# Performance work log

Measured on AMD Instinct MI355X. Metric: run time of the kernel, lower is better.

## Reference

```python
import jax, jax.numpy as jnp
import numpy as np

C = 64          # channel multiplicity of node irreps (64x0e + 64x1o)
N = 10000       # nodes
E = 160000      # edges
F_EDGE = 8      # edge radial features (8x0e)
N_ELEM = 10     # one-hot element types (node_attrs, unused by this block)
WNUM = 4 * C    # conv_tp.weight_numel: 4 uvu instructions x 64 channels
SQ3 = float(np.sqrt(3.0))


def split_feats(x):
    # e3nn flat layout: [64 scalars | 64 vectors x 3 (u-major)]
    s = x[:, :C]
    v = x[:, C:].reshape(-1, C, 3)
    return s, v


def o3_linear(s, v, W0, W1):
    # per-irrep channel mixing with 1/sqrt(fan_in) normalization
    inv = 1.0 / float(np.sqrt(C))
    return (s @ W0) * inv, jnp.einsum('ncm,cd->ndm', v, W1) * inv


def fc_net(x, ws):
    # e3nn FullyConnectedNet: silu MLP with 1/sqrt(fan_in) scaling, no act on last
    for w in ws[:-1]:
        x = jax.nn.silu((x @ w) / float(np.sqrt(w.shape[0])))
    w = ws[-1]
    return (x @ w) / float(np.sqrt(w.shape[0]))


def setup_inputs() -> dict:
    key = jax.random.key(0)
    ks = jax.random.split(key, 16)
    inp = {}
    inp['node_attrs'] = jax.random.normal(ks[0], (N, N_ELEM), jnp.float32)
    inp['node_feats'] = jax.random.normal(ks[1], (N, C + 3 * C), jnp.float32)
    inp['edge_attrs'] = jax.random.normal(ks[2], (E, 4), jnp.float32)
    inp['edge_feats'] = jax.random.normal(ks[3], (E, F_EDGE), jnp.float32)
    inp['edge_index'] = jax.random.randint(ks[4], (2, E), 0, N, jnp.int32)
    inp['edge_vectors'] = jax.random.normal(ks[5], (E, 3), jnp.float32)
    inp['batch'] = jax.random.randint(ks[6], (N,), 0, 16, jnp.int32)
    inp['num_graphs'] = 16
    # learned params
    inp['W1_0'] = jax.random.normal(ks[7], (C, C), jnp.float32)
    inp['W1_1'] = jax.random.normal(ks[8], (C, C), jnp.float32)
    inp['W2_0'] = jax.random.normal(ks[9], (C, C), jnp.float32)
    inp['W2_1'] = jax.random.normal(ks[10], (C, C), jnp.float32)
    inp['fc_w0'] = jax.random.normal(ks[11], (F_EDGE, 64), jnp.float32)
    inp['fc_w1'] = jax.random.normal(ks[12], (64, 64), jnp.float32)
    inp['fc_w2'] = jax.random.normal(ks[13], (64, 64), jnp.float32)
    inp['fc_w3'] = jax.random.normal(ks[14], (64, WNUM), jnp.float32)
    k15, k16 = jax.random.split(ks[15])
    inp['Wf'] = jax.random.normal(k15, (2 * C, 1), jnp.float32)   # 128x0e mid -> 1x0e
    inp['Wm1'] = jax.random.normal(k16, (C, 1), jnp.float32)      # 64x1o -> 1x1o multipole
    return inp


def reference(node_attrs, node_feats, edge_attrs, edge_feats, edge_index,
              edge_vectors, batch, num_graphs,
              W1_0, W1_1, W2_0, W2_1, fc_w0, fc_w1, fc_w2, fc_w3, Wf, Wm1):
    sender = edge_index[0]
    receiver = edge_index[1]

    # per-edge tensor-product weights from radial features: [E, 4*C]
    tp_w = fc_net(edge_feats, [fc_w0, fc_w1, fc_w2, fc_w3])
    w0, w1, w2, w3 = (tp_w[:, 0 * C:1 * C], tp_w[:, 1 * C:2 * C],
                      tp_w[:, 2 * C:3 * C], tp_w[:, 3 * C:4 * C])

    s, v = split_feats(node_feats)
    s1, v1 = o3_linear(s, v, W1_0, W1_1)
    s2, v2 = o3_linear(s, v, W2_0, W2_1)

    # gather + symmetric bond features
    bs = s1[sender] + s2[receiver]          # [E, C] scalars
    bv = v1[sender] + v2[receiver]          # [E, C, 3] vectors

    y0 = edge_attrs[:, 0]                   # l=0 edge attr
    y1 = edge_attrs[:, 1:4]                 # l=1 edge attr

    # CG tensor product (uvu, shared_weights=False): only scalar (0e) outputs of
    # irreps_mid reach the final 1x0e o3.Linear, so the 1o paths drop out exactly.
    m0a = w0 * bs * y0[:, None]                                  # 0e x 0e -> 0e
    m0b = w3 * (jnp.einsum('ecm,em->ec', bv, y1) / SQ3)          # 1o x 1o -> 0e

    # final o3.Linear (128x0e -> 1x0e) and /40 scaling
    mid0 = jnp.concatenate([m0a, m0b], axis=-1)                  # [E, 2C]
    p_ji = (mid0 @ Wf)[:, 0] / float(np.sqrt(2 * C)) / 40.0      # [E]

    # double scatter-sum: antisymmetric charge transfer
    charges = (jax.ops.segment_sum(p_ji, receiver, num_segments=N)
               - jax.ops.segment_sum(p_ji, sender, num_segments=N))

    # multipole block: 0e component zeroed then overwritten by charges
    mvec = jnp.einsum('ncm,cd->ndm', v, Wm1)[:, 0, :] / float(np.sqrt(C))  # [N, 3]
    multipoles = jnp.concatenate([charges[:, None], mvec], axis=-1)        # [N, 4]

    return multipoles, p_ji[:, None]
```

## Files before the change

### kernel.cpp

```cpp
#include <hip/hip_runtime.h>
#include <hip/hip_bf16.h>

typedef float v4f __attribute__((ext_vector_type(4)));
typedef float f32x4 __attribute__((ext_vector_type(4)));
typedef unsigned short u16;
typedef unsigned short us4 __attribute__((ext_vector_type(4)));
typedef unsigned short us8 __attribute__((ext_vector_type(8)));
typedef short s16x8 __attribute__((ext_vector_type(8)));

#define N_NODES 10000
#define N_EDGES 160000

#define SWZ(idx, row) ((idx) ^ (((row) & 7) << 3))
#define GIDX(r, o) (((r) << 8) + (((((o) >> 3) ^ ((r) & 7))) << 3) + ((o) & 7))

__device__ __forceinline__ u16 f2b(float x) {
  union { float f; unsigned u; } v; v.f = x;
  unsigned r = v.u + 0x7fffu + ((v.u >> 16) & 1u);
  return (u16)(r >> 16);
}
__device__ __forceinline__ float b2f(u16 u) {
  union { unsigned u; float f; } v; v.u = ((unsigned)u) << 16; return v.f;
}
__device__ __forceinline__ float silu_f(float x) { return x / (1.0f + __expf(-x)); }

__device__ __forceinline__ void bar_lgkm() {
  asm volatile("s_waitcnt lgkmcnt(0)" ::: "memory");
  __builtin_amdgcn_s_barrier();
}

__device__ __forceinline__ void gload_lds16(const u16* g, u16* l) {
  __builtin_amdgcn_global_load_lds(
      (const __attribute__((address_space(1))) unsigned int*)g,
      (__attribute__((address_space(3))) unsigned int*)l, 16, 0, 0);
}

__global__ __launch_bounds__(256) void prep_kernel(
    const float* __restrict__ fcw1, const float* __restrict__ fcw2,
    const float* __restrict__ fcw3,
    const float* __restrict__ W10, const float* __restrict__ W20,
    const float* __restrict__ W11, const float* __restrict__ W21,
    u16* __restrict__ prep, float* __restrict__ out)
{
  const int fid = blockIdx.x * 256 + threadIdx.x;
  for (int i = fid; i < N_NODES; i += 4096) out[(size_t)i * 4] = 0.f;
  int f, sec;
  if (fid < 512)       { sec = 0; f = fid; }
  else if (fid < 1024) { sec = 1; f = fid - 512; }
  else if (fid < 2048) { sec = 2; f = fid - 1024; }
  else if (fid < 3072) { sec = 3; f = fid - 2048; }
  else                 { sec = 4; f = fid - 3072; }
  const int lane = f & 63, kw = (f >> 6) & 1, ut = f >> 7;
  us8 vals;
  #pragma unroll
  for (int j = 0; j < 8; ++j) {
    const int k = kw * 32 + (lane >> 4) * 8 + j;
    float v;
    if (sec == 0) v = fcw1[k * 64 + ut * 16 + (lane & 15)];
    else if (sec == 1) v = fcw2[k * 64 + ut * 16 + (lane & 15)];
    else if (sec == 2) {
      const int col = (ut < 4) ? (ut * 16 + (lane & 15)) : (192 + (ut - 4) * 16 + (lane & 15));
      v = fcw3[k * 256 + col];
    } else if (sec == 3) {
      const int u = ut * 16 + (lane & 15);
      v = (u < 64) ? W10[k * 64 + u] : W20[k * 64 + (u - 64)];
    } else {
      const int u = ut * 16 + (lane & 15);
      v = (u < 64) ? W11[k * 64 + u] : W21[k * 64 + (u - 64)];
    }
    vals[j] = f2b(v);
  }
  *(us8*)&prep[(size_t)fid * 8] = vals;
}

__global__ __launch_bounds__(256) void node_kernel(
    const float* __restrict__ nf,
    const u16* __restrict__ prepNS, const u16* __restrict__ prepNV,
    const float* __restrict__ Wm1,
    u16* __restrict__ Atab, u16* __restrict__ Btab, float* __restrict__ out)
{
  __shared__ u16 Ss[1024];
  __shared__ u16 Vs[3][1024];
  const int tid = threadIdx.x, w = tid >> 6, lane = tid & 63;
  const int nb = blockIdx.x;

  #pragma unroll
  for (int it = 0; it < 4; ++it) {
    const int flat = it * 1024 + tid * 4;
    const int nl = flat >> 8;
    const int col = flat & 255;
    const v4f x = *(const v4f*)&nf[((size_t)(nb * 16 + nl)) * 256 + col];
    #pragma unroll
    for (int i = 0; i < 4; ++i) {
      const int c2 = col + i;
      const u16 b = f2b(x[i]);
      if (c2 < 64) Ss[SWZ(nl * 64 + c2, nl)] = b;
      else {
        const int cc = c2 - 64, c = cc / 3, m = cc - c * 3;
        Vs[m][SWZ(nl * 64 + c, nl)] = b;
      }
    }
  }
  __syncthreads();

  const int nr = lane & 15, kg = (lane >> 4) * 8;
  const u16* plane = (w == 0) ? Ss : Vs[w - 1];
  const u16* pw = (w == 0) ? prepNS : prepNV;
  const s16x8 b0 = *(const s16x8*)&plane[SWZ(nr * 64 + kg, nr)];
  const s16x8 b1 = *(const s16x8*)&plane[SWZ(nr * 64 + 32 + kg, nr)];
  const int node = nb * 16 + nr;
  #pragma unroll
  for (int utg = 0; utg < 8; ++utg) {
    const s16x8 a0 = *(const s16x8*)&pw[((utg * 2 + 0) * 64 + lane) * 8];
    const s16x8 a1 = *(const s16x8*)&pw[((utg * 2 + 1) * 64 + lane) * 8];
    f32x4 acc = {0.f, 0.f, 0.f, 0.f};
    acc = __builtin_amdgcn_mfma_f32_16x16x32_bf16(a0, b0, acc, 0, 0, 0);
    acc = __builtin_amdgcn_mfma_f32_16x16x32_bf16(a1, b1, acc, 0, 0, 0);
    us4 st;
    #pragma unroll
    for (int j = 0; j < 4; ++j) st[j] = f2b(acc[j] * 0.125f);
    u16* tab = (utg < 4) ? Atab : Btab;
    const int ch = w * 64 + (utg & 3) * 16 + (lane >> 4) * 4;
    *(us4*)&tab[(size_t)node * 256 + ch] = st;
  }

  if (tid < 48) {
    const int nl3 = tid / 3, m = tid - nl3 * 3;
    float acc = 0.f;
    #pragma unroll 8
    for (int c = 0; c < 64; ++c)
      acc += b2f(Vs[m][SWZ(nl3 * 64 + c, nl3)]) * Wm1[c];
    out[(nb * 16 + nl3) * 4 + 1 + m] = acc * 0.125f;
  }
}

__device__ __forceinline__ void mfma_layer32(const u16* Hin, u16* Hout,
                                             s16x8 a0, s16x8 a1, int w, int lane) {
  const int er = lane & 15, kg = (lane >> 4) * 8;
  #pragma unroll
  for (int et = 0; et < 2; ++et) {
    const int e = et * 16 + er;
    const s16x8 b0 = *(const s16x8*)&Hin[SWZ(e * 64 + kg, e)];
    const s16x8 b1 = *(const s16x8*)&Hin[SWZ(e * 64 + 32 + kg, e)];
    f32x4 acc = {0.f, 0.f, 0.f, 0.f};
    acc = __builtin_amdgcn_mfma_f32_16x16x32_bf16(a0, b0, acc, 0, 0, 0);
    acc = __builtin_amdgcn_mfma_f32_16x16x32_bf16(a1, b1, acc, 0, 0, 0);
    us4 st;
    #pragma unroll
    for (int j = 0; j < 4; ++j) st[j] = f2b(silu_f(acc[j] * 0.125f));
    *(us4*)&Hout[SWZ(e * 64 + w * 16 + (lane >> 4) * 4, e)] = st;
  }
}

__global__ __launch_bounds__(256, 2) void edge_kernel(
    const float* __restrict__ edge_attrs,
    const float* __restrict__ edge_feats,
    const int*   __restrict__ edge_index,
    const float* __restrict__ fcw0,
    const u16*   __restrict__ prep,
    const float* __restrict__ Wf,
    const u16*   __restrict__ Atab, const u16* __restrict__ Btab,
    float* __restrict__ out, float* __restrict__ p_out)
{
  __shared__ u16 G[2][16384];
  __shared__ u16 HA[2048], HB[2048];
  __shared__ float F[256];
  __shared__ float W0L[512];
  __shared__ float yL[4][32];
  __shared__ float Psum[128];

  const int tid = threadIdx.x, w = tid >> 6, lane = tid & 63;
  const int half = lane >> 5, l31 = lane & 31;
  const int er = lane & 15, kg = (lane >> 4) * 8;
  const int cb = w * 16 + (lane >> 4) * 4;
  const int eb0 = blockIdx.x * 128;

  const u16* pL2 = prep;
  const u16* pL3 = prep + 512 * 8;
  const u16* pL4 = prep + 1024 * 8;
  const s16x8 a2_0 = *(const s16x8*)&pL2[((w * 2 + 0) * 64 + lane) * 8];
  const s16x8 a2_1 = *(const s16x8*)&pL2[((w * 2 + 1) * 64 + lane) * 8];
  const s16x8 a3_0 = *(const s16x8*)&pL3[((w * 2 + 0) * 64 + lane) * 8];
  const s16x8 a3_1 = *(const s16x8*)&pL3[((w * 2 + 1) * 64 + lane) * 8];
  const s16x8 as0 = *(const s16x8*)&pL4[((w * 2 + 0) * 64 + lane) * 8];
  const s16x8 as1 = *(const s16x8*)&pL4[((w * 2 + 1) * 64 + lane) * 8];
  const s16x8 av0 = *(const s16x8*)&pL4[(((4 + w) * 2 + 0) * 64 + lane) * 8];
  const s16x8 av1 = *(const s16x8*)&pL4[(((4 + w) * 2 + 1) * 64 + lane) * 8];
  const v4f wfA = *(const v4f*)&Wf[cb];
  v4f wfB = *(const v4f*)&Wf[64 + cb];
  #pragma unroll
  for (int j = 0; j < 4; ++j) wfB[j] *= 0.5773502691896258f;
  W0L[tid] = fcw0[tid]; W0L[256 + tid] = fcw0[256 + tid];

  const u16* tabW = (w < 2) ? Atab : Btab;
  const int  eoff = (w < 2) ? 0 : N_EDGES;

  int nidx[2][8];
  int sndR[2], rcvR[2];
  v4f eaR[2], f0R[2], f1R[2];

  {
    #pragma unroll
    for (int i = 0; i < 8; ++i)
      nidx[0][i] = edge_index[eoff + eb0 + (w & 1) * 16 + 2 * i + half];
    if (tid < 32) {
      sndR[0] = edge_index[eb0 + tid];
      rcvR[0] = edge_index[N_EDGES + eb0 + tid];
      eaR[0] = *(const v4f*)&edge_attrs[(size_t)(eb0 + tid) * 4];
      f0R[0] = *(const v4f*)&edge_feats[(size_t)(eb0 + tid) * 8];
      f1R[0] = *(const v4f*)&edge_feats[(size_t)(eb0 + tid) * 8 + 4];
    }
    asm volatile("s_waitcnt vmcnt(0)" ::: "memory");
    #pragma unroll
    for (int i = 0; i < 8; ++i) {
      const int grow = w * 16 + 2 * i + half;
      const u16* src = tabW + (size_t)nidx[0][i] * 256 + (size_t)((l31 ^ (grow & 7)) << 3);
      gload_lds16(src, &G[0][(w * 16 + 2 * i) * 256]);
    }
    __builtin_amdgcn_sched_barrier(0);
    if (tid < 32) {
      yL[0][tid] = eaR[0][0]; yL[1][tid] = eaR[0][1];
      yL[2][tid] = eaR[0][2]; yL[3][tid] = eaR[0][3];
      #pragma unroll
      for (int k = 0; k < 4; ++k) {
        F[k * 32 + tid] = f0R[0][k]; F[(k + 4) * 32 + tid] = f1R[0][k];
      }
    }
    bar_lgkm();
  }

  #pragma unroll
  for (int t = 0; t < 4; ++t) {
    const int cur = t & 1, nxt = cur ^ 1;
    const int eb = eb0 + t * 32;

    if (t < 3) {
      const int ebn = eb + 32;
      #pragma unroll
      for (int i = 0; i < 8; ++i)
        nidx[nxt][i] = edge_index[eoff + ebn + (w & 1) * 16 + 2 * i + half];
      if (tid < 32) {
        sndR[nxt] = edge_index[ebn + tid];
        rcvR[nxt] = edge_index[N_EDGES + ebn + tid];
        eaR[nxt] = *(const v4f*)&edge_attrs[(size_t)(ebn + tid) * 4];
        f0R[nxt] = *(const v4f*)&edge_feats[(size_t)(ebn + tid) * 8];
        f1R[nxt] = *(const v4f*)&edge_feats[(size_t)(ebn + tid) * 8 + 4];
      }
      __builtin_amdgcn_sched_barrier(0);
    }

    {
      const int u0 = w * 16 + half * 8;
      float acc[8] = {0.f,0.f,0.f,0.f,0.f,0.f,0.f,0.f};
      #pragma unroll
      for (int k = 0; k < 8; ++k) {
        const float fv = F[k * 32 + l31];
        #pragma unroll
        for (int q = 0; q < 2; ++q) {
          const v4f wr = *(const v4f*)&W0L[k * 64 + u0 + q * 4];
          #pragma unroll
          for (int j = 0; j < 4; ++j) acc[q * 4 + j] += fv * wr[j];
        }
      }
      us8 o;
      #pragma unroll
      for (int j = 0; j < 8; ++j) o[j] = f2b(silu_f(acc[j] * 0.35355339059327373f));
      *(us8*)&HA[SWZ(l31 * 64 + u0, l31)] = o;
    }
    bar_lgkm();
    mfma_layer32(HA, HB, a2_0, a2_1, w, lane);
    bar_lgkm();
    mfma_layer32(HB, HA, a3_0, a3_1, w, lane);
    bar_lgkm();

    f32x4 accS[2], accV[2];
    #pragma unroll
    for (int et = 0; et < 2; ++et) {
      const int e = et * 16 + er;
      const s16x8 b0 = *(const s16x8*)&HA[SWZ(e * 64 + kg, e)];
      const s16x8 b1 = *(const s16x8*)&HA[SWZ(e * 64 + 32 + kg, e)];
      f32x4 aS = {0.f,0.f,0.f,0.f}, aV = {0.f,0.f,0.f,0.f};
      aS = __builtin_amdgcn_mfma_f32_16x16x32_bf16(as0, b0, aS, 0, 0, 0);
      aS = __builtin_amdgcn_mfma_f32_16x16x32_bf16(as1, b1, aS, 0, 0, 0);
      aV = __builtin_amdgcn_mfma_f32_16x16x32_bf16(av0, b0, aV, 0, 0, 0);
      aV = __builtin_amdgcn_mfma_f32_16x16x32_bf16(av1, b1, aV, 0, 0, 0);
      accS[et] = aS; accV[et] = aV;
    }

    asm volatile("s_waitcnt vmcnt(0)" ::: "memory");
    if (t < 3) {
      #pragma unroll
      for (int i = 0; i < 8; ++i) {
        const int grow = w * 16 + 2 * i + half;
        const u16* src = tabW + (size_t)nidx[nxt][i] * 256 + (size_t)((l31 ^ (grow & 7)) << 3);
        gload_lds16(src, &G[nxt][(w * 16 + 2 * i) * 256]);
      }
      __builtin_amdgcn_sched_barrier(0);
    }
    __builtin_amdgcn_s_barrier();

    #pragma unroll
    for (int et = 0; et < 2; ++et) {
      const int e = et * 16 + er;
      const int rA = e, rB = 32 + e;
      const us4 As = *(const us4*)&G[cur][GIDX(rA, cb)];
      const us4 Ax = *(const us4*)&G[cur][GIDX(rA, 64 + cb)];
      const us4 Ay = *(const us4*)&G[cur][GIDX(rA, 128 + cb)];
      const us4 Az = *(const us4*)&G[cur][GIDX(rA, 192 + cb)];
      const us4 Bs = *(const us4*)&G[cur][GIDX(rB, cb)];
      const us4 Bx = *(const us4*)&G[cur][GIDX(rB, 64 + cb)];
      const us4 By = *(const us4*)&G[cur][GIDX(rB, 128 + cb)];
      const us4 Bz = *(const us4*)&G[cur][GIDX(rB, 192 + cb)];
      const float y0 = yL[0][e], yx = yL[1][e], yy = yL[2][e], yz = yL[3][e];
      float part = 0.f;
      #pragma unroll
      for (int j = 0; j < 4; ++j) {
        const float bs = b2f(As[j]) + b2f(Bs[j]);
        const float bv = (b2f(Ax[j]) + b2f(Bx[j])) * yx +
                         (b2f(Ay[j]) + b2f(By[j])) * yy +
                         (b2f(Az[j]) + b2f(Bz[j])) * yz;
        part += accS[et][j] * bs * y0 * wfA[j] + accV[et][j] * bv * wfB[j];
      }
      part += __shfl_xor(part, 16);
      part += __shfl_xor(part, 32);
      if (lane < 16) Psum[w * 32 + et * 16 + lane] = part;
    }
    bar_lgkm();
    if (tid < 32) {
      const float p = (Psum[tid] + Psum[32 + tid] + Psum[64 + tid] + Psum[96 + tid])
                      * 2.7621358640766505e-4f;
      p_out[eb + tid] = p;
      atomicAdd(&out[(size_t)rcvR[cur] * 4], p);
      atomicAdd(&out[(size_t)sndR[cur] * 4], -p);
      if (t < 3) {
        yL[0][tid] = eaR[nxt][0]; yL[1][tid] = eaR[nxt][1];
        yL[2][tid] = eaR[nxt][2]; yL[3][tid] = eaR[nxt][3];
        #pragma unroll
        for (int k = 0; k < 4; ++k) {
          F[k * 32 + tid] = f0R[nxt][k]; F[(k + 4) * 32 + tid] = f1R[nxt][k];
        }
      }
    }
    bar_lgkm();
  }
}

extern "C" void kernel_launch(void* const* d_in, const int* in_sizes, int n_in,
                              void* d_out, int out_size, void* d_ws, size_t ws_size,
                              hipStream_t stream) {
  const float* node_feats = (const float*)d_in[1];
  const float* edge_attrs = (const float*)d_in[2];
  const float* edge_feats = (const float*)d_in[3];
  const int*   edge_index = (const int*)d_in[4];
  const float* W10  = (const float*)d_in[8];
  const float* W11  = (const float*)d_in[9];
  const float* W20  = (const float*)d_in[10];
  const float* W21  = (const float*)d_in[11];
  const float* fcw0 = (const float*)d_in[12];
  const float* fcw1 = (const float*)d_in[13];
  const float* fcw2 = (const float*)d_in[14];
  const float* fcw3 = (const float*)d_in[15];
  const float* Wf   = (const float*)d_in[16];
  const float* Wm1  = (const float*)d_in[17];
  float* out = (float*)d_out;

  char* ws = (char*)d_ws;
  u16* Atab = (u16*)ws;
  u16* Btab = (u16*)(ws + 5120000);
  u16* prep = (u16*)(ws + 10240000);

  prep_kernel<<<16, 256, 0, stream>>>(fcw1, fcw2, fcw3, W10, W20, W11, W21,
                                      prep, out);
  node_kernel<<<625, 256, 0, stream>>>(node_feats, prep + 2048 * 8, prep + 3072 * 8,
                                       Wm1, Atab, Btab, out);
  edge_kernel<<<1250, 256, 0, stream>>>(edge_attrs, edge_feats, edge_index,
                                        fcw0, prep, Wf, Atab, Btab,
                                        out, out + 40000);
}
```

Baseline: 153.1 us.

## Single-buffer edge gather LDS to raise occupancy, double tiles per block

The edge kernel's gather buffer goes from double to single buffered, roughly halving its shared memory footprint, and launch bounds are raised from 2 to 3 blocks per CU. The next tile's gather is now issued after the current tile's reads finish instead of overlapping with its MLP. Each block now handles 8 tiles of 32 edges, so the grid shrinks to 625 blocks. The aim is to hide gather latency through occupancy rather than in-block prefetch, at the cost of losing that intra-block overlap and having fewer blocks. The node kernel's multipole dot product is also spread over 4 lanes with shuffle reduction and Wm1 staged in LDS.

```diff
diff --git a/kernel.cpp b/kernel.cpp
--- a/kernel.cpp
+++ b/kernel.cpp
@@ -10,6 +10,7 @@
 
 #define N_NODES 10000
 #define N_EDGES 160000
+#define NTILE 8
 
 #define SWZ(idx, row) ((idx) ^ (((row) & 7) << 3))
 #define GIDX(r, o) (((r) << 8) + (((((o) >> 3) ^ ((r) & 7))) << 3) + ((o) & 7))
@@ -81,9 +82,11 @@
 {
   __shared__ u16 Ss[1024];
   __shared__ u16 Vs[3][1024];
+  __shared__ float wm1s[64];
   const int tid = threadIdx.x, w = tid >> 6, lane = tid & 63;
   const int nb = blockIdx.x;
 
+  if (tid < 64) wm1s[tid] = Wm1[tid];
   #pragma unroll
   for (int it = 0; it < 4; ++it) {
     const int flat = it * 1024 + tid * 4;
@@ -124,13 +127,18 @@
     *(us4*)&tab[(size_t)node * 256 + ch] = st;
   }
 
-  if (tid < 48) {
-    const int nl3 = tid / 3, m = tid - nl3 * 3;
+  if (tid < 192) {
+    const int task = tid >> 2, sub = tid & 3;
+    const int nl3 = task / 3, m = task - nl3 * 3;
     float acc = 0.f;
-    #pragma unroll 8
-    for (int c = 0; c < 64; ++c)
-      acc += b2f(Vs[m][SWZ(nl3 * 64 + c, nl3)]) * Wm1[c];
-    out[(nb * 16 + nl3) * 4 + 1 + m] = acc * 0.125f;
+    #pragma unroll
+    for (int i = 0; i < 16; ++i) {
+      const int c = sub * 16 + i;
+      acc += b2f(Vs[m][SWZ(nl3 * 64 + c, nl3)]) * wm1s[c];
+    }
+    acc += __shfl_xor(acc, 1);
+    acc += __shfl_xor(acc, 2);
+    if (sub == 0) out[(nb * 16 + nl3) * 4 + 1 + m] = acc * 0.125f;
   }
 }
 
@@ -152,7 +160,7 @@
   }
 }
 
-__global__ __launch_bounds__(256, 2) void edge_kernel(
+__global__ __launch_bounds__(256, 3) void edge_kernel(
     const float* __restrict__ edge_attrs,
     const float* __restrict__ edge_feats,
     const int*   __restrict__ edge_index,
@@ -162,7 +170,7 @@
     const u16*   __restrict__ Atab, const u16* __restrict__ Btab,
     float* __restrict__ out, float* __restrict__ p_out)
 {
-  __shared__ u16 G[2][16384];
+  __shared__ u16 G[16384];
   __shared__ u16 HA[2048], HB[2048];
   __shared__ float F[256];
   __shared__ float W0L[512];
@@ -173,7 +181,7 @@
   const int half = lane >> 5, l31 = lane & 31;
   const int er = lane & 15, kg = (lane >> 4) * 8;
   const int cb = w * 16 + (lane >> 4) * 4;
-  const int eb0 = blockIdx.x * 128;
+  const int eb0 = blockIdx.x * (NTILE * 32);
 
   const u16* pL2 = prep;
   const u16* pL3 = prep + 512 * 8;
@@ -215,7 +223,7 @@
     for (int i = 0; i < 8; ++i) {
       const int grow = w * 16 + 2 * i + half;
       const u16* src = tabW + (size_t)nidx[0][i] * 256 + (size_t)((l31 ^ (grow & 7)) << 3);
-      gload_lds16(src, &G[0][(w * 16 + 2 * i) * 256]);
+      gload_lds16(src, &G[(w * 16 + 2 * i) * 256]);
     }
     __builtin_amdgcn_sched_barrier(0);
     if (tid < 32) {
@@ -230,11 +238,11 @@
   }
 
   #pragma unroll
-  for (int t = 0; t < 4; ++t) {
+  for (int t = 0; t < NTILE; ++t) {
     const int cur = t & 1, nxt = cur ^ 1;
     const int eb = eb0 + t * 32;
 
-    if (t < 3) {
+    if (t < NTILE - 1) {
       const int ebn = eb + 32;
       #pragma unroll
       for (int i = 0; i < 8; ++i)
@@ -288,29 +296,20 @@
     }
 
     asm volatile("s_waitcnt vmcnt(0)" ::: "memory");
-    if (t < 3) {
-      #pragma unroll
-      for (int i = 0; i < 8; ++i) {
-        const int grow = w * 16 + 2 * i + half;
-        const u16* src = tabW + (size_t)nidx[nxt][i] * 256 + (size_t)((l31 ^ (grow & 7)) << 3);
-        gload_lds16(src, &G[nxt][(w * 16 + 2 * i) * 256]);
-      }
-      __builtin_amdgcn_sched_barrier(0);
-    }
     __builtin_amdgcn_s_barrier();
 
     #pragma unroll
     for (int et = 0; et < 2; ++et) {
       const int e = et * 16 + er;
       const int rA = e, rB = 32 + e;
-      const us4 As = *(const us4*)&G[cur][GIDX(rA, cb)];
-      const us4 Ax = *(const us4*)&G[cur][GIDX(rA, 64 + cb)];
-      const us4 Ay = *(const us4*)&G[cur][GIDX(rA, 128 + cb)];
-      const us4 Az = *(const us4*)&G[cur][GIDX(rA, 192 + cb)];
-      const us4 Bs = *(const us4*)&G[cur][GIDX(rB, cb)];
-      const us4 Bx = *(const us4*)&G[cur][GIDX(rB, 64 + cb)];
-      const us4 By = *(const us4*)&G[cur][GIDX(rB, 128 + cb)];
-      const us4 Bz = *(const us4*)&G[cur][GIDX(rB, 192 + cb)];
+      const us4 As = *(const us4*)&G[GIDX(rA, cb)];
+      const us4 Ax = *(const us4*)&G[GIDX(rA, 64 + cb)];
+      const us4 Ay = *(const us4*)&G[GIDX(rA, 128 + cb)];
+      const us4 Az = *(const us4*)&G[GIDX(rA, 192 + cb)];
+      const us4 Bs = *(const us4*)&G[GIDX(rB, cb)];
+      const us4 Bx = *(const us4*)&G[GIDX(rB, 64 + cb)];
+      const us4 By = *(const us4*)&G[GIDX(rB, 128 + cb)];
+      const us4 Bz = *(const us4*)&G[GIDX(rB, 192 + cb)];
       const float y0 = yL[0][e], yx = yL[1][e], yy = yL[2][e], yz = yL[3][e];
       float part = 0.f;
       #pragma unroll
@@ -326,13 +325,24 @@
       if (lane < 16) Psum[w * 32 + et * 16 + lane] = part;
     }
     bar_lgkm();
+
+    if (t < NTILE - 1) {
+      #pragma unroll
+      for (int i = 0; i < 8; ++i) {
+        const int grow = w * 16 + 2 * i + half;
+        const u16* src = tabW + (size_t)nidx[nxt][i] * 256 + (size_t)((l31 ^ (grow & 7)) << 3);
+        gload_lds16(src, &G[(w * 16 + 2 * i) * 256]);
+      }
+      __builtin_amdgcn_sched_barrier(0);
+    }
+
     if (tid < 32) {
       const float p = (Psum[tid] + Psum[32 + tid] + Psum[64 + tid] + Psum[96 + tid])
                       * 2.7621358640766505e-4f;
       p_out[eb + tid] = p;
       atomicAdd(&out[(size_t)rcvR[cur] * 4], p);
       atomicAdd(&out[(size_t)sndR[cur] * 4], -p);
-      if (t < 3) {
+      if (t < NTILE - 1) {
         yL[0][tid] = eaR[nxt][0]; yL[1][tid] = eaR[nxt][1];
         yL[2][tid] = eaR[nxt][2]; yL[3][tid] = eaR[nxt][3];
         #pragma unroll
@@ -373,7 +383,7 @@
                                       prep, out);
   node_kernel<<<625, 256, 0, stream>>>(node_feats, prep + 2048 * 8, prep + 3072 * 8,
                                        Wm1, Atab, Btab, out);
-  edge_kernel<<<1250, 256, 0, stream>>>(edge_attrs, edge_feats, edge_index,
-                                        fcw0, prep, Wf, Atab, Btab,
-                                        out, out + 40000);
-}
+  edge_kernel<<<625, 256, 0, stream>>>(edge_attrs, edge_feats, edge_index,
+                                       fcw0, prep, Wf, Atab, Btab,
+                                       out, out + 40000);
+}
```

After: 161.9 us. +5.7%, slower.

## Move first radial MLP layer to MFMA and parallelize multipole dot product

Applied to the files above, without the earlier changes.

Replaces the scalar FMA loop for the first fc_net layer (8->64) with a bf16 MFMA, zero-padding K from 8 to 32. The prep kernel packs fcw0 into the MFMA operand layout, and edge features are staged to LDS as bf16. It also wraps the MFMA sections in s_setprio to favour matrix issue, and splits the node multipole dot product across 4 lanes with shuffle reduction, reading Wm1 from LDS. Rounding the first-layer inputs and weights to bf16 adds some precision loss.

```diff
diff --git a/kernel.cpp b/kernel.cpp
--- a/kernel.cpp
+++ b/kernel.cpp
@@ -36,6 +36,7 @@
 }
 
 __global__ __launch_bounds__(256) void prep_kernel(
+    const float* __restrict__ fcw0,
     const float* __restrict__ fcw1, const float* __restrict__ fcw2,
     const float* __restrict__ fcw3,
     const float* __restrict__ W10, const float* __restrict__ W20,
@@ -43,32 +44,43 @@
     u16* __restrict__ prep, float* __restrict__ out)
 {
   const int fid = blockIdx.x * 256 + threadIdx.x;
-  for (int i = fid; i < N_NODES; i += 4096) out[(size_t)i * 4] = 0.f;
+  for (int i = fid; i < N_NODES; i += 4352) out[(size_t)i * 4] = 0.f;
   int f, sec;
   if (fid < 512)       { sec = 0; f = fid; }
   else if (fid < 1024) { sec = 1; f = fid - 512; }
   else if (fid < 2048) { sec = 2; f = fid - 1024; }
   else if (fid < 3072) { sec = 3; f = fid - 2048; }
-  else                 { sec = 4; f = fid - 3072; }
-  const int lane = f & 63, kw = (f >> 6) & 1, ut = f >> 7;
+  else if (fid < 4096) { sec = 4; f = fid - 3072; }
+  else                 { sec = 5; f = fid - 4096; }
+  const int lane = f & 63;
   us8 vals;
-  #pragma unroll
-  for (int j = 0; j < 8; ++j) {
-    const int k = kw * 32 + (lane >> 4) * 8 + j;
-    float v;
-    if (sec == 0) v = fcw1[k * 64 + ut * 16 + (lane & 15)];
-    else if (sec == 1) v = fcw2[k * 64 + ut * 16 + (lane & 15)];
-    else if (sec == 2) {
-      const int col = (ut < 4) ? (ut * 16 + (lane & 15)) : (192 + (ut - 4) * 16 + (lane & 15));
-      v = fcw3[k * 256 + col];
-    } else if (sec == 3) {
-      const int u = ut * 16 + (lane & 15);
-      v = (u < 64) ? W10[k * 64 + u] : W20[k * 64 + (u - 64)];
-    } else {
-      const int u = ut * 16 + (lane & 15);
-      v = (u < 64) ? W11[k * 64 + u] : W21[k * 64 + (u - 64)];
-    }
-    vals[j] = f2b(v);
+  if (sec == 5) {
+    const int ut = f >> 6;
+    #pragma unroll
+    for (int j = 0; j < 8; ++j) {
+      const int k = (lane >> 4) * 8 + j;
+      vals[j] = (k < 8) ? f2b(fcw0[k * 64 + ut * 16 + (lane & 15)]) : (u16)0;
+    }
+  } else {
+    const int kw = (f >> 6) & 1, ut = f >> 7;
+    #pragma unroll
+    for (int j = 0; j < 8; ++j) {
+      const int k = kw * 32 + (lane >> 4) * 8 + j;
+      float v;
+      if (sec == 0) v = fcw1[k * 64 + ut * 16 + (lane & 15)];
+      else if (sec == 1) v = fcw2[k * 64 + ut * 16 + (lane & 15)];
+      else if (sec == 2) {
+        const int col = (ut < 4) ? (ut * 16 + (lane & 15)) : (192 + (ut - 4) * 16 + (lane & 15));
+        v = fcw3[k * 256 + col];
+      } else if (sec == 3) {
+        const int u = ut * 16 + (lane & 15);
+        v = (u < 64) ? W10[k * 64 + u] : W20[k * 64 + (u - 64)];
+      } else {
+        const int u = ut * 16 + (lane & 15);
+        v = (u < 64) ? W11[k * 64 + u] : W21[k * 64 + (u - 64)];
+      }
+      vals[j] = f2b(v);
+    }
   }
   *(us8*)&prep[(size_t)fid * 8] = vals;
 }
@@ -81,9 +93,11 @@
 {
   __shared__ u16 Ss[1024];
   __shared__ u16 Vs[3][1024];
+  __shared__ float wm1s[64];
   const int tid = threadIdx.x, w = tid >> 6, lane = tid & 63;
   const int nb = blockIdx.x;
 
+  if (tid < 64) wm1s[tid] = Wm1[tid];
   #pragma unroll
   for (int it = 0; it < 4; ++it) {
     const int flat = it * 1024 + tid * 4;
@@ -124,19 +138,25 @@
     *(us4*)&tab[(size_t)node * 256 + ch] = st;
   }
 
-  if (tid < 48) {
-    const int nl3 = tid / 3, m = tid - nl3 * 3;
+  if (tid < 192) {
+    const int task = tid >> 2, sub = tid & 3;
+    const int nl3 = task / 3, m = task - nl3 * 3;
     float acc = 0.f;
-    #pragma unroll 8
-    for (int c = 0; c < 64; ++c)
-      acc += b2f(Vs[m][SWZ(nl3 * 64 + c, nl3)]) * Wm1[c];
-    out[(nb * 16 + nl3) * 4 + 1 + m] = acc * 0.125f;
+    #pragma unroll
+    for (int i = 0; i < 16; ++i) {
+      const int c = sub * 16 + i;
+      acc += b2f(Vs[m][SWZ(nl3 * 64 + c, nl3)]) * wm1s[c];
+    }
+    acc += __shfl_xor(acc, 1);
+    acc += __shfl_xor(acc, 2);
+    if (sub == 0) out[(nb * 16 + nl3) * 4 + 1 + m] = acc * 0.125f;
   }
 }
 
 __device__ __forceinline__ void mfma_layer32(const u16* Hin, u16* Hout,
                                              s16x8 a0, s16x8 a1, int w, int lane) {
   const int er = lane & 15, kg = (lane >> 4) * 8;
+  __builtin_amdgcn_s_setprio(1);
   #pragma unroll
   for (int et = 0; et < 2; ++et) {
     const int e = et * 16 + er;
@@ -150,13 +170,13 @@
     for (int j = 0; j < 4; ++j) st[j] = f2b(silu_f(acc[j] * 0.125f));
     *(us4*)&Hout[SWZ(e * 64 + w * 16 + (lane >> 4) * 4, e)] = st;
   }
+  __builtin_amdgcn_s_setprio(0);
 }
 
 __global__ __launch_bounds__(256, 2) void edge_kernel(
     const float* __restrict__ edge_attrs,
     const float* __restrict__ edge_feats,
     const int*   __restrict__ edge_index,
-    const float* __restrict__ fcw0,
     const u16*   __restrict__ prep,
     const float* __restrict__ Wf,
     const u16*   __restrict__ Atab, const u16* __restrict__ Btab,
@@ -164,8 +184,7 @@
 {
   __shared__ u16 G[2][16384];
   __shared__ u16 HA[2048], HB[2048];
-  __shared__ float F[256];
-  __shared__ float W0L[512];
+  __shared__ u16 F16[256];
   __shared__ float yL[4][32];
   __shared__ float Psum[128];
 
@@ -186,11 +205,11 @@
   const s16x8 as1 = *(const s16x8*)&pL4[((w * 2 + 1) * 64 + lane) * 8];
   const s16x8 av0 = *(const s16x8*)&pL4[(((4 + w) * 2 + 0) * 64 + lane) * 8];
   const s16x8 av1 = *(const s16x8*)&pL4[(((4 + w) * 2 + 1) * 64 + lane) * 8];
+  const s16x8 a1w = *(const s16x8*)&prep[(size_t)(4096 + w * 64 + lane) * 8];
   const v4f wfA = *(const v4f*)&Wf[cb];
   v4f wfB = *(const v4f*)&Wf[64 + cb];
   #pragma unroll
   for (int j = 0; j < 4; ++j) wfB[j] *= 0.5773502691896258f;
-  W0L[tid] = fcw0[tid]; W0L[256 + tid] = fcw0[256 + tid];
 
   const u16* tabW = (w < 2) ? Atab : Btab;
   const int  eoff = (w < 2) ? 0 : N_EDGES;
@@ -221,10 +240,10 @@
     if (tid < 32) {
       yL[0][tid] = eaR[0][0]; yL[1][tid] = eaR[0][1];
       yL[2][tid] = eaR[0][2]; yL[3][tid] = eaR[0][3];
-      #pragma unroll
-      for (int k = 0; k < 4; ++k) {
-        F[k * 32 + tid] = f0R[0][k]; F[(k + 4) * 32 + tid] = f1R[0][k];
-      }
+      us8 o;
+      #pragma unroll
+      for (int k = 0; k < 4; ++k) { o[k] = f2b(f0R[0][k]); o[4 + k] = f2b(f1R[0][k]); }
+      *(us8*)&F16[tid * 8] = o;
     }
     bar_lgkm();
   }
@@ -250,22 +269,21 @@
     }
 
     {
-      const int u0 = w * 16 + half * 8;
-      float acc[8] = {0.f,0.f,0.f,0.f,0.f,0.f,0.f,0.f};
-      #pragma unroll
-      for (int k = 0; k < 8; ++k) {
-        const float fv = F[k * 32 + l31];
+      __builtin_amdgcn_s_setprio(1);
+      #pragma unroll
+      for (int et = 0; et < 2; ++et) {
+        s16x8 bF = {0, 0, 0, 0, 0, 0, 0, 0};
+        if (lane < 16) bF = *(const s16x8*)&F16[(et * 16 + lane) * 8];
+        f32x4 acc = {0.f, 0.f, 0.f, 0.f};
+        acc = __builtin_amdgcn_mfma_f32_16x16x32_bf16(a1w, bF, acc, 0, 0, 0);
+        const int e = et * 16 + er;
+        us4 st;
         #pragma unroll
-        for (int q = 0; q < 2; ++q) {
-          const v4f wr = *(const v4f*)&W0L[k * 64 + u0 + q * 4];
-          #pragma unroll
-          for (int j = 0; j < 4; ++j) acc[q * 4 + j] += fv * wr[j];
-        }
-      }
-      us8 o;
-      #pragma unroll
-      for (int j = 0; j < 8; ++j) o[j] = f2b(silu_f(acc[j] * 0.35355339059327373f));
-      *(us8*)&HA[SWZ(l31 * 64 + u0, l31)] = o;
+        for (int j = 0; j < 4; ++j)
+          st[j] = f2b(silu_f(acc[j] * 0.35355339059327373f));
+        *(us4*)&HA[SWZ(e * 64 + w * 16 + (lane >> 4) * 4, e)] = st;
+      }
+      __builtin_amdgcn_s_setprio(0);
     }
     bar_lgkm();
     mfma_layer32(HA, HB, a2_0, a2_1, w, lane);
@@ -274,6 +292,7 @@
     bar_lgkm();
 
     f32x4 accS[2], accV[2];
+    __builtin_amdgcn_s_setprio(1);
     #pragma unroll
     for (int et = 0; et < 2; ++et) {
       const int e = et * 16 + er;
@@ -286,6 +305,7 @@
       aV = __builtin_amdgcn_mfma_f32_16x16x32_bf16(av1, b1, aV, 0, 0, 0);
       accS[et] = aS; accV[et] = aV;
     }
+    __builtin_amdgcn_s_setprio(0);
 
     asm volatile("s_waitcnt vmcnt(0)" ::: "memory");
     if (t < 3) {
@@ -335,10 +355,10 @@
       if (t < 3) {
         yL[0][tid] = eaR[nxt][0]; yL[1][tid] = eaR[nxt][1];
         yL[2][tid] = eaR[nxt][2]; yL[3][tid] = eaR[nxt][3];
+        us8 o;
         #pragma unroll
-        for (int k = 0; k < 4; ++k) {
-          F[k * 32 + tid] = f0R[nxt][k]; F[(k + 4) * 32 + tid] = f1R[nxt][k];
-        }
+        for (int k = 0; k < 4; ++k) { o[k] = f2b(f0R[nxt][k]); o[4 + k] = f2b(f1R[nxt][k]); }
+        *(us8*)&F16[tid * 8] = o;
       }
     }
     bar_lgkm();
@@ -369,11 +389,11 @@
   u16* Btab = (u16*)(ws + 5120000);
   u16* prep = (u16*)(ws + 10240000);
 
-  prep_kernel<<<16, 256, 0, stream>>>(fcw1, fcw2, fcw3, W10, W20, W11, W21,
+  prep_kernel<<<17, 256, 0, stream>>>(fcw0, fcw1, fcw2, fcw3, W10, W20, W11, W21,
                                       prep, out);
   node_kernel<<<625, 256, 0, stream>>>(node_feats, prep + 2048 * 8, prep + 3072 * 8,
                                        Wm1, Atab, Btab, out);
   edge_kernel<<<1250, 256, 0, stream>>>(edge_attrs, edge_feats, edge_index,
-                                        fcw0, prep, Wf, Atab, Btab,
+                                        prep, Wf, Atab, Btab,
                                         out, out + 40000);
 }
```

Result: slower. 156.3 us (+2.1%).
